# Optimization experiments

Hardware: AMD Instinct MI355X
Metric: run time of the kernel (lower is better)

The kernel has to match this reference:

```python
import jax, jax.numpy as jnp
import numpy as np

NEG = -1e30  # effective -inf that stays stable in fp32 log-sum-exp
BLANK = 0


def _lse3(a, b, c):
    m = jnp.maximum(jnp.maximum(a, b), c)
    return m + jnp.log(jnp.exp(a - m) + jnp.exp(b - m) + jnp.exp(c - m))


def _ctc_loss_sum(log_probs, input_lengths, targets, target_lengths):
    # log_probs: [B, T, V] already log-softmaxed; targets: [B, S] int, blank=0
    B, T, V = log_probs.shape
    S = targets.shape[1]
    L = 2 * S + 1  # extended label seq: blank-interleaved

    ext = jnp.full((B, L), BLANK, dtype=targets.dtype)
    ext = ext.at[:, 1::2].set(targets)  # [B, L]

    # gather per-frame log-probs of extended labels: [B, T, L]
    lp_ext = jnp.take_along_axis(
        log_probs, jnp.broadcast_to(ext[:, None, :], (B, T, L)), axis=2)

    # skip transition s-2 -> s allowed iff ext[s] != blank and ext[s] != ext[s-2]
    ext_prev2 = jnp.pad(ext[:, :-2], ((0, 0), (2, 0)), constant_values=BLANK)
    can_skip = (ext != BLANK) & (ext != ext_prev2) & (jnp.arange(L)[None, :] >= 2)

    # alpha init at t=0
    alpha = jnp.full((B, L), NEG, dtype=log_probs.dtype)
    alpha = alpha.at[:, 0].set(lp_ext[:, 0, 0])
    alpha = alpha.at[:, 1].set(lp_ext[:, 0, 1])

    lp_seq = jnp.swapaxes(lp_ext, 0, 1)[1:]          # [T-1, B, L]
    valid = jnp.arange(1, T)[:, None] < input_lengths[None, :]  # [T-1, B]

    def step(a, xs):
        lp_t, v = xs  # [B, L], [B]
        a1 = jnp.pad(a[:, :-1], ((0, 0), (1, 0)), constant_values=NEG)
        a2 = jnp.pad(a[:, :-2], ((0, 0), (2, 0)), constant_values=NEG)
        a2 = jnp.where(can_skip, a2, NEG)
        new = _lse3(a, a1, a2) + lp_t
        a = jnp.where(v[:, None], new, a)  # freeze past each utterance's length
        return a, None

    alpha, _ = jax.lax.scan(step, alpha, (lp_seq, valid))

    # terminal states: last blank (2*tl) and last label (2*tl - 1)
    end = 2 * target_lengths.astype(jnp.int32)
    aT = jnp.take_along_axis(alpha, jnp.stack([end, end - 1], axis=1), axis=1)  # [B, 2]
    ll = jax.scipy.special.logsumexp(aT, axis=1)
    loss = -ll
    loss = jnp.where(loss > 1e29, 0.0, loss)  # zero_infinity=True
    return jnp.sum(loss)  # reduction='sum'


def setup_inputs() -> dict:
    B, T, V, S = 64, 1024, 512, 128
    key = jax.random.key(0)
    k1, k2, k3, k4 = jax.random.split(key, 4)
    output_tensor = jax.random.normal(k1, (B, T, V), dtype=jnp.float32)
    output_lengths = jax.random.randint(k2, (B,), T // 2, T + 1, dtype=jnp.int32)
    target_tensor = jax.random.randint(k3, (B, S), 1, V, dtype=jnp.int32)  # no blanks
    target_lengths = jax.random.randint(k4, (B,), S // 2, S + 1, dtype=jnp.int32)
    return {"output_tensor": output_tensor, "output_lengths": output_lengths,
            "target_tensor": target_tensor, "target_lengths": target_lengths}


def reference(output_tensor, output_lengths, target_tensor, target_lengths):
    log_probs = jax.nn.log_softmax(output_tensor, axis=2)
    return _ctc_loss_sum(log_probs, output_lengths, target_tensor, target_lengths)
```

## Files before the change

kernel.cpp:

```cpp
#include <hip/hip_runtime.h>
#include <cstdint>

#define T_LEN 1024
#define V_DIM 512
#define S_LEN 128
#define NEG2  (-1.0e30f)

__device__ float2 g_plab[(size_t)64 * T_LEN * 64];
__device__ float  g_pblank[(size_t)64 * T_LEN];

__global__ __launch_bounds__(256) void ctc_prep(
    const float* __restrict__ x, const int* __restrict__ lens,
    const int* __restrict__ tgts)
{
    const int lane = threadIdx.x & 63;
    const int wid  = (int)((blockIdx.x * blockDim.x + threadIdx.x) >> 6);
    const int b = wid >> 10;
    const int t = wid & (T_LEN - 1);
    if (t >= lens[b]) return;

    const float* row = x + (size_t)wid * V_DIM;
    const float4 u = *(const float4*)(row + lane * 8);
    const float4 v = *(const float4*)(row + lane * 8 + 4);

    float m = fmaxf(fmaxf(fmaxf(u.x, u.y), fmaxf(u.z, u.w)),
                    fmaxf(fmaxf(v.x, v.y), fmaxf(v.z, v.w)));
    #pragma unroll
    for (int d = 32; d; d >>= 1) m = fmaxf(m, __shfl_xor(m, d));

    const float L2E = 1.44269504088896340736f;
    float s = exp2f((u.x - m) * L2E) + exp2f((u.y - m) * L2E)
            + exp2f((u.z - m) * L2E) + exp2f((u.w - m) * L2E)
            + exp2f((v.x - m) * L2E) + exp2f((v.y - m) * L2E)
            + exp2f((v.z - m) * L2E) + exp2f((v.w - m) * L2E);
    #pragma unroll
    for (int d = 32; d; d >>= 1) s += __shfl_xor(s, d);

    const float off = m * L2E + log2f(s);

    if (lane == 0) g_pblank[wid] = exp2f(row[0] * L2E - off);

    const int2 tg = *(const int2*)(tgts + b * S_LEN + 2 * lane);
    g_plab[(size_t)wid * 64 + lane] =
        make_float2(exp2f(row[tg.x] * L2E - off), exp2f(row[tg.y] * L2E - off));
}

struct AlphaState {
    float a0, a1, a2, a3, a4;
    int C;
};

static __device__ __forceinline__ void alpha_step(
    AlphaState& st, float pb, float2 lp, bool cs1, bool cs3, int lane)
{
    const float p3 = __shfl_up(st.a3, 1);
    const int   Cp = __shfl_up(st.C, 1);
    const float ssum = ((st.a0 + st.a1) + (st.a2 + st.a3)) + st.a4;
    const int   Cn = (ssum == 0.f) ? Cp : st.C;
    int e = 127 + (Cp - Cn);
    e = e < 0 ? 0 : (e > 252 ? 252 : e);
    const float adj = __int_as_float((unsigned)e << 23);
    const float p3v = (lane == 0) ? 0.f : p3 * adj;
    const float n0 = (st.a0 + p3v) * pb;
    const float n1 = ((st.a1 + st.a0) + (cs1 ? p3v : 0.f)) * lp.x;
    const float n2 = (st.a2 + st.a1) * pb;
    const float n3 = ((st.a3 + st.a2) + (cs3 ? st.a1 : 0.f)) * lp.y;
    const float n4 = (st.a4 + st.a3) * pb;
    st.a0 = n0; st.a1 = n1; st.a2 = n2; st.a3 = n3; st.a4 = n4; st.C = Cn;
}

static __device__ __forceinline__ void alpha_rescale(AlphaState& st)
{
    const float mx = fmaxf(fmaxf(fmaxf(st.a0, st.a1), fmaxf(st.a2, st.a3)), st.a4);
    const int ee = (__float_as_int(mx) >> 23) & 255;
    const bool ok = (ee > 0) && (ee < 255);
    const float sc = ok ? __int_as_float((unsigned)(254 - ee) << 23) : 1.0f;
    const int dC = ok ? (ee - 127) : 0;
    st.a0 *= sc; st.a1 *= sc; st.a2 *= sc; st.a3 *= sc; st.a4 *= sc; st.C += dC;
}

__global__ __launch_bounds__(64) void ctc_alpha(
    const int* __restrict__ lens, const int* __restrict__ tgts,
    const int* __restrict__ tlens, float* __restrict__ out)
{
    const int b    = blockIdx.x;
    const int lane = threadIdx.x;
    const int len  = lens[b];
    const int tl   = tlens[b];
    const int lenm1 = len - 1;

    const int tA = tgts[b * S_LEN + 2 * lane];
    const int tB = tgts[b * S_LEN + 2 * lane + 1];
    const int tPrev = __shfl_up(tB, 1);
    const bool cs1 = (lane > 0) && (tA != tPrev);
    const bool cs3 = (tB != tA);

    const size_t rowb = (size_t)b * T_LEN;
    const float*  __restrict__ pb_b = g_pblank + rowb;
    const float2* __restrict__ pl_b = g_plab + rowb * 64;

    AlphaState st;
    st.a0 = 0.f; st.a1 = 0.f; st.a2 = 0.f; st.a3 = 0.f; st.a4 = 0.f; st.C = 0;
    if (lane == 0) { st.a0 = pb_b[0]; st.a1 = pl_b[0].x; }

    const int D = 16;
    float  pbA[D], pbB[D];
    float2 plA[D], plB[D];

    #pragma unroll
    for (int i = 0; i < D; ++i) {
        const int t = 1 + i;
        const int tt = (t < lenm1) ? t : lenm1;
        pbA[i] = pb_b[tt];
        plA[i] = pl_b[(size_t)tt * 64 + lane];
    }

    int t0 = 1;
    for (; t0 + D <= len; t0 += D) {
        #pragma unroll
        for (int i = 0; i < D; ++i) {
            const int tp = t0 + D + i;
            const int tt = (tp < lenm1) ? tp : lenm1;
            pbB[i] = pb_b[tt];
            plB[i] = pl_b[(size_t)tt * 64 + lane];
        }
        #pragma unroll
        for (int i = 0; i < D; ++i) {
            alpha_step(st, pbA[i], plA[i], cs1, cs3, lane);
            if ((i & 3) == 3) alpha_rescale(st);
        }
        #pragma unroll
        for (int i = 0; i < D; ++i) { pbA[i] = pbB[i]; plA[i] = plB[i]; }
    }
    #pragma unroll
    for (int i = 0; i < D; ++i) {
        if (t0 + i < len) {
            alpha_step(st, pbA[i], plA[i], cs1, cs3, lane);
            if ((i & 3) == 3) alpha_rescale(st);
        }
    }

    const int end = 2 * tl;
    float v1, v2; int C1, C2;
    {
        int s = end;
        int lsrc = s >> 2; if (lsrc > 63) lsrc = 63;
        const int slot = s & 3;
        float cand = (slot == 0) ? st.a0 : (slot == 1) ? st.a1
                   : (slot == 2) ? st.a2 : st.a3;
        if (s == 256) cand = st.a4;
        v1 = __shfl(cand, lsrc);
        C1 = __shfl(st.C, lsrc);

        s = end - 1;
        lsrc = s >> 2;
        const int slot2 = s & 3;
        cand = (slot2 == 0) ? st.a0 : (slot2 == 1) ? st.a1
             : (slot2 == 2) ? st.a2 : st.a3;
        v2 = __shfl(cand, lsrc);
        C2 = __shfl(st.C, lsrc);
    }
    const float l1 = (v1 > 0.f) ? log2f(v1) + (float)C1 : NEG2;
    const float l2 = (v2 > 0.f) ? log2f(v2) + (float)C2 : NEG2;
    const float mM = fmaxf(l1, l2);
    const float ll2 = mM + log2f(exp2f(l1 - mM) + exp2f(l2 - mM));
    float loss = -ll2 * 0.69314718055994530942f;
    if (!(loss < 1e29f)) loss = 0.f;
    if (lane == 0) atomicAdd(out, loss);
}

extern "C" void kernel_launch(void* const* d_in, const int* in_sizes, int n_in,
                              void* d_out, int out_size, void* d_ws, size_t ws_size,
                              hipStream_t stream) {
    const float* x     = (const float*)d_in[0];
    const int*   lens  = (const int*)d_in[1];
    const int*   tgts  = (const int*)d_in[2];
    const int*   tlens = (const int*)d_in[3];
    float* out = (float*)d_out;

    hipMemsetAsync(d_out, 0, (size_t)out_size * sizeof(float), stream);
    ctc_prep<<<(64 * T_LEN) / 4, 256, 0, stream>>>(x, lens, tgts);
    ctc_alpha<<<64, 64, 0, stream>>>(lens, tgts, tlens, out);
}
```

Before: 303.8 us.

## Double-buffer label probabilities into LDS via async global_load_lds in alpha kernel

Replaces the register-based prefetch of per-frame label and blank probabilities with a double-buffered LDS pipeline: label probs are DMA'd into shared memory with global_load_lds one chunk ahead, and all blank probs are staged into LDS up front. The chunk size grows from 16 to 32 frames. This aims to hide global-memory latency in the serial alpha recursion and free registers. It relies on a raw waitcnt encoding and a padded global buffer for overreads, and there is no barrier between the DMA writes and the LDS reads, so ordering within the single wave is assumed.

```diff
diff --git a/kernel.cpp b/kernel.cpp
--- a/kernel.cpp
+++ b/kernel.cpp
@@ -5,9 +5,17 @@
 #define V_DIM 512
 #define S_LEN 128
 #define NEG2  (-1.0e30f)
+#define CH    32
 
-__device__ float2 g_plab[(size_t)64 * T_LEN * 64];
+__device__ float2 g_plab[(size_t)64 * T_LEN * 64 + 64];
 __device__ float  g_pblank[(size_t)64 * T_LEN];
+
+static __device__ __forceinline__ void dma16(const void* g, void* l) {
+    __builtin_amdgcn_global_load_lds(
+        (const __attribute__((address_space(1))) unsigned int*)g,
+        (__attribute__((address_space(3))) unsigned int*)l,
+        16, 0, 0);
+}
 
 __global__ __launch_bounds__(256) void ctc_prep(
     const float* __restrict__ x, const int* __restrict__ lens,
@@ -45,10 +53,7 @@
         make_float2(exp2f(row[tg.x] * L2E - off), exp2f(row[tg.y] * L2E - off));
 }
 
-struct AlphaState {
-    float a0, a1, a2, a3, a4;
-    int C;
-};
+struct AlphaState { float a0, a1, a2, a3, a4; int C; };
 
 static __device__ __forceinline__ void alpha_step(
     AlphaState& st, float pb, float2 lp, bool cs1, bool cs3, int lane)
@@ -83,6 +88,9 @@
     const int* __restrict__ lens, const int* __restrict__ tgts,
     const int* __restrict__ tlens, float* __restrict__ out)
 {
+    __shared__ float  lds_pb[T_LEN];
+    __shared__ float2 lds_pl[2][CH * 64];
+
     const int b    = blockIdx.x;
     const int lane = threadIdx.x;
     const int len  = lens[b];
@@ -99,45 +107,48 @@
     const float*  __restrict__ pb_b = g_pblank + rowb;
     const float2* __restrict__ pl_b = g_plab + rowb * 64;
 
+    #pragma unroll
+    for (int j = 0; j < CH / 2; ++j) {
+        const int r = 1 + 2 * j;
+        dma16(pl_b + (size_t)r * 64 + lane * 2, &lds_pl[0][j * 128]);
+    }
+
+    #pragma unroll
+    for (int k = 0; k < T_LEN / 64; ++k)
+        lds_pb[k * 64 + lane] = pb_b[k * 64 + lane];
+
     AlphaState st;
     st.a0 = 0.f; st.a1 = 0.f; st.a2 = 0.f; st.a3 = 0.f; st.a4 = 0.f; st.C = 0;
     if (lane == 0) { st.a0 = pb_b[0]; st.a1 = pl_b[0].x; }
 
-    const int D = 16;
-    float  pbA[D], pbB[D];
-    float2 plA[D], plB[D];
-
-    #pragma unroll
-    for (int i = 0; i < D; ++i) {
-        const int t = 1 + i;
-        const int tt = (t < lenm1) ? t : lenm1;
-        pbA[i] = pb_b[tt];
-        plA[i] = pl_b[(size_t)tt * 64 + lane];
-    }
-
+    int buf = 0;
     int t0 = 1;
-    for (; t0 + D <= len; t0 += D) {
+    for (; t0 + CH <= len; t0 += CH) {
+        __builtin_amdgcn_s_waitcnt(0x0F70);
+        float2 pl[CH];
         #pragma unroll
-        for (int i = 0; i < D; ++i) {
-            const int tp = t0 + D + i;
-            const int tt = (tp < lenm1) ? tp : lenm1;
-            pbB[i] = pb_b[tt];
-            plB[i] = pl_b[(size_t)tt * 64 + lane];
+        for (int i = 0; i < CH; ++i)
+            pl[i] = lds_pl[buf][i * 64 + lane];
+        #pragma unroll
+        for (int j = 0; j < CH / 2; ++j) {
+            int r = t0 + CH + 2 * j;
+            r = (r < lenm1) ? r : lenm1;
+            dma16(pl_b + (size_t)r * 64 + lane * 2, &lds_pl[buf ^ 1][j * 128]);
         }
         #pragma unroll
-        for (int i = 0; i < D; ++i) {
-            alpha_step(st, pbA[i], plA[i], cs1, cs3, lane);
+        for (int i = 0; i < CH; ++i) {
+            const float pb = lds_pb[t0 + i];
+            alpha_step(st, pb, pl[i], cs1, cs3, lane);
             if ((i & 3) == 3) alpha_rescale(st);
         }
-        #pragma unroll
-        for (int i = 0; i < D; ++i) { pbA[i] = pbB[i]; plA[i] = plB[i]; }
+        buf ^= 1;
     }
-    #pragma unroll
-    for (int i = 0; i < D; ++i) {
-        if (t0 + i < len) {
-            alpha_step(st, pbA[i], plA[i], cs1, cs3, lane);
-            if ((i & 3) == 3) alpha_rescale(st);
-        }
+    __builtin_amdgcn_s_waitcnt(0x0F70);
+    for (int i = 0; t0 + i < len; ++i) {
+        const float2 plv = lds_pl[buf][i * 64 + lane];
+        const float  pb  = lds_pb[t0 + i];
+        alpha_step(st, pb, plv, cs1, cs3, lane);
+        if ((i & 3) == 3) alpha_rescale(st);
     }
 
     const int end = 2 * tl;
```

Result: faster. 294.1 us (-3.2%).
